# Performance work log

Hardware: AMD Instinct MI355X
Metric: run time of the kernel (lower is better)

## Reference

```python
import jax, jax.numpy as jnp
import numpy as np

# SwitchNet f* dims
B = 1024
Nb1, Nw1 = 8, 10          # input: Nb1^2=64 blocks, window 2*Nw1^2=200
Nb2x, Nb2y = 8, 8
Nw2x, Nw2y = 10, 10
R = 16
J1 = Nb1 * Nb1            # 64
K1 = 2 * Nw1 * Nw1        # 200
L1 = Nb2x * Nb2y * R      # 1024
J2 = Nb2x * Nb2y * J1     # 4096
J3 = Nb2x * Nb2y          # 64
K3 = J1 * R               # 1024
L3 = 2 * Nw2x * Nw2y      # 200


def _dm(x, kernel, bias):
    # per-block batched GEMM: x [B, J, K] @ kernel [J, K, L] + bias [1, J, L]
    return jnp.einsum('ijk,jkl->ijl', x, kernel) + bias


def setup_inputs() -> dict:
    key = jax.random.key(0)
    ks = jax.random.split(key, 7)
    u = lambda k, shape: jax.random.uniform(k, shape, dtype=jnp.float32) * 0.01
    return {
        'x': jax.random.normal(ks[0], (B, Nb1 * Nw1 * Nb1 * Nw1, 2), dtype=jnp.float32),
        'k1': u(ks[1], (J1, K1, L1)),
        'b1': u(ks[2], (1, J1, L1)),
        'k2': u(ks[3], (J2, R, R)),
        'b2': u(ks[4], (1, J2, R)),
        'k3': u(ks[5], (J3, K3, L3)),
        'b3': u(ks[6], (1, J3, L3)),
    }


def reference(x, k1, b1, k2, b2, k3, b3):
    bs = x.shape[0]
    # gather input windows: [B, Nb1, Nw1, Nb1, Nw1, 2] -> block-major
    h = x.reshape(bs, Nb1, Nw1, Nb1, Nw1, 2)
    h = h.transpose(0, 1, 3, 2, 4, 5)
    h = h.reshape(bs, J1, K1)
    h = _dm(h, k1, b1)                                   # [B, 64, 1024]
    h = h.reshape(bs, J1, Nb2x * Nb2y, R)
    h = h.transpose(0, 3, 1, 2)                          # [B, r, 64, 64]
    h = h.reshape(bs, J2, R)
    h = _dm(h, k2, b2)                                   # [B, 4096, r]
    h = h.reshape(bs, J3, K3)
    h = _dm(h, k3, b3)                                   # [B, 64, 200]
    h = h.reshape(bs, Nb2x, Nb2y, Nw2x, Nw2y, 2)
    h = h.transpose(0, 1, 3, 2, 4, 5)
    return h.reshape(bs, Nb2x * Nw2x, Nb2y * Nw2y, 2)   # [B, 80, 80, 2]
```

## Files before the change

kernel.cpp:

```cpp
#include <hip/hip_runtime.h>

typedef __attribute__((ext_vector_type(8))) short short8;
typedef __attribute__((ext_vector_type(4))) short bfx4;
typedef __attribute__((ext_vector_type(4))) float floatx4;

__device__ __forceinline__ float bf2f(short u) {
  unsigned int i = ((unsigned int)(unsigned short)u) << 16;
  return __builtin_bit_cast(float, i);
}
__device__ __forceinline__ short f2bf(float f) {
  unsigned int x = __builtin_bit_cast(unsigned int, f);
  x += 0x7fffu + ((x >> 16) & 1u);
  return (short)(x >> 16);
}

__device__ __forceinline__ void gl_lds16(const short* g, short* lds) {
  __builtin_amdgcn_global_load_lds(
      (const __attribute__((address_space(1))) unsigned int*)g,
      (__attribute__((address_space(3))) unsigned int*)lds, 16, 0, 0);
}

#define BC 256

__global__ __launch_bounds__(256) void gather_x(const float* __restrict__ x,
                                                short* __restrict__ hA, int bOffset) {
  int tid = blockIdx.x * 256 + threadIdx.x;
  const int total = 64 * BC * 112;
  if (tid >= total) return;
  int kp2 = tid % 112;
  int rem = tid / 112;
  int b_loc = rem & (BC - 1);
  int j1 = rem / BC;
  unsigned int pair = 0;
  if (kp2 < 100) {
    int wx = kp2 / 10;
    int wy = kp2 - wx * 10;
    int bx = j1 >> 3, by = j1 & 7;
    const float* p = x + (size_t)(bOffset + b_loc) * 12800 +
                     ((size_t)(bx * 800 + wx * 80 + by * 10 + wy)) * 2;
    float2 v = *(const float2*)p;
    pair = ((unsigned int)(unsigned short)f2bf(v.x)) |
           (((unsigned int)(unsigned short)f2bf(v.y)) << 16);
  }
  *(unsigned int*)&hA[rem * 224 + kp2 * 2] = pair;
}

__global__ __launch_bounds__(256) void transpose_k1(const float* __restrict__ k1,
                                                    short* __restrict__ k1t) {
  const int j1 = blockIdx.x;
  const int nBase = blockIdx.y * 64;
  const int kBase = blockIdx.z * 56;
  __shared__ short tr[64][68];
  const int t = threadIdx.x;
  const int nl = t & 63;
  const int ksub = t >> 6;
  const float* src = k1 + (size_t)j1 * 204800 + (size_t)kBase * 1024 + nBase + nl;
#pragma unroll
  for (int pass = 0; pass < 14; ++pass) {
    int kloc = pass * 4 + ksub;
    int k = kBase + kloc;
    tr[nl][kloc] = (k < 200) ? f2bf(src[kloc * 1024]) : (short)0;
  }
  __syncthreads();
  short* dstbase = k1t + ((size_t)j1 * 1024 + nBase) * 224 + kBase;
#pragma unroll
  for (int p = 0; p < 4; ++p) {
    int u = p * 256 + t;
    int row = u >> 4;
    int kq = u & 15;
    if (kq < 14) {
      bfx4 v = *(const bfx4*)&tr[row][kq * 4];
      *(bfx4*)&dstbase[row * 224 + kq * 4] = v;
    }
  }
}

__global__ __launch_bounds__(256) void transpose_k3(const float* __restrict__ k3,
                                                    short* __restrict__ k3t) {
  const int j3 = blockIdx.x;
  const int kBase = blockIdx.y * 128;
  const int nBase = blockIdx.z * 64;
  __shared__ short tr[64][132];
  const int t = threadIdx.x;
  const int nl = t & 63;
  const int ksub = t >> 6;
  const int nGlob = nBase + nl;
  const bool valid = (nGlob < 200);
  const float* src = k3 + (size_t)j3 * 204800 + (size_t)kBase * 200 + nGlob;
#pragma unroll 4
  for (int pass = 0; pass < 32; ++pass) {
    int k = pass * 4 + ksub;
    tr[nl][k] = valid ? f2bf(src[k * 200]) : (short)0;
  }
  __syncthreads();
  short* dstbase = k3t + ((size_t)j3 * 256 + nBase) * 1024 + kBase;
#pragma unroll
  for (int pass = 0; pass < 8; ++pass) {
    int idx = (pass * 256 + t) * 4;
    int row = idx >> 7;
    int koff = idx & 127;
    bfx4 v = *(const bfx4*)&tr[row][koff];
    *(bfx4*)&dstbase[row * 1024 + koff] = v;
  }
}

__global__ __launch_bounds__(256) void gemm_stage1(const short* __restrict__ hA,
                                                   const short* __restrict__ k1t,
                                                   const float* __restrict__ b1,
                                                   short* __restrict__ h1) {
  int bid = (int)blockIdx.x + 8 * (int)blockIdx.y + 16 * (int)blockIdx.z;
  bid = ((bid & 7) << 7) | (bid >> 3);
  const int nBase = (bid & 7) * 128;
  const int mBase = ((bid >> 3) & 1) * 128;
  const int j1 = bid >> 4;
  __shared__ short As[128 * 64];
  __shared__ short Bs[128 * 64];
  const int tid = threadIdx.x;
  const int lane = tid & 63;
  const int wave = tid >> 6;
  const int quad = lane >> 4;
  const int l16 = lane & 15;
  const int wm = wave >> 1, wn = wave & 1;
  const int sRow = tid >> 3;
  const int sCol = ((tid & 7) ^ (sRow & 7)) * 8;
  const short* Aj = hA + (size_t)j1 * BC * 224 + (size_t)(mBase + sRow) * 224 + sCol;
  const short* Bj =
      k1t + (size_t)j1 * 1024 * 224 + (size_t)(nBase + sRow) * 224 + sCol;
  const int tRow = tid >> 2;
  const int tCol = (tid & 3) * 8;
  const short* Ajt =
      hA + (size_t)j1 * BC * 224 + (size_t)(mBase + tRow) * 224 + 192 + tCol;
  const short* Bjt =
      k1t + (size_t)j1 * 1024 * 224 + (size_t)(nBase + tRow) * 224 + 192 + tCol;
  short* ldsA = &As[tid * 8];
  short* ldsB = &Bs[tid * 8];
  floatx4 acc[4][4] = {};

  for (int kk = 0; kk < 192; kk += 64) {
    __syncthreads();
#pragma unroll
    for (int c = 0; c < 4; ++c) {
      gl_lds16(Aj + c * 32 * 224 + kk, ldsA + c * 2048);
      gl_lds16(Bj + c * 32 * 224 + kk, ldsB + c * 2048);
    }
    __syncthreads();
#pragma unroll
    for (int ks = 0; ks < 2; ++ks) {
      short8 af[4], bfv[4];
#pragma unroll
      for (int mt = 0; mt < 4; ++mt) {
        int r = wm * 64 + mt * 16 + l16;
        af[mt] = *(const short8*)&As[r * 64 + ((ks * 4 + quad) ^ (l16 & 7)) * 8];
      }
#pragma unroll
      for (int nt = 0; nt < 4; ++nt) {
        int r = wn * 64 + nt * 16 + l16;
        bfv[nt] = *(const short8*)&Bs[r * 64 + ((ks * 4 + quad) ^ (l16 & 7)) * 8];
      }
#pragma unroll
      for (int mt = 0; mt < 4; ++mt)
#pragma unroll
        for (int nt = 0; nt < 4; ++nt)
          acc[mt][nt] = __builtin_amdgcn_mfma_f32_16x16x32_bf16(af[mt], bfv[nt],
                                                                acc[mt][nt], 0, 0, 0);
    }
  }
  __syncthreads();
  gl_lds16(Ajt, ldsA);
  gl_lds16(Ajt + 64 * 224, ldsA + 2048);
  gl_lds16(Bjt, ldsB);
  gl_lds16(Bjt + 64 * 224, ldsB + 2048);
  __syncthreads();
  {
    short8 af[4], bfv[4];
#pragma unroll
    for (int mt = 0; mt < 4; ++mt)
      af[mt] = *(const short8*)&As[(wm * 64 + mt * 16 + l16) * 32 + quad * 8];
#pragma unroll
    for (int nt = 0; nt < 4; ++nt)
      bfv[nt] = *(const short8*)&Bs[(wn * 64 + nt * 16 + l16) * 32 + quad * 8];
#pragma unroll
    for (int mt = 0; mt < 4; ++mt)
#pragma unroll
      for (int nt = 0; nt < 4; ++nt)
        acc[mt][nt] = __builtin_amdgcn_mfma_f32_16x16x32_bf16(af[mt], bfv[nt],
                                                              acc[mt][nt], 0, 0, 0);
  }
#pragma unroll
  for (int nt = 0; nt < 4; ++nt) {
    int n = nBase + wn * 64 + nt * 16 + l16;
    float bias = b1[j1 * 1024 + n];
#pragma unroll
    for (int mt = 0; mt < 4; ++mt) {
#pragma unroll
      for (int r = 0; r < 4; ++r) {
        int m = mBase + wm * 64 + mt * 16 + quad * 4 + r;
        h1[((size_t)j1 * BC + m) * 1024 + n] = f2bf(acc[mt][nt][r] + bias);
      }
    }
  }
}

__global__ __launch_bounds__(256) void stage2(const short* __restrict__ h1,
                                              const float* __restrict__ k2,
                                              const float* __restrict__ b2,
                                              short* __restrict__ h2p, int mTot,
                                              int bOff2) {
  const int j1 = blockIdx.x;
  const int bBase = blockIdx.y * 8;
  __shared__ short in_s[8][1024];
  __shared__ short w_s[256 * 66];
  __shared__ float bias_s[16 * 64];
  const int tid = threadIdx.x;
#pragma unroll
  for (int ii = 0; ii < 4; ++ii) {
    int flat = (ii * 256 + tid) * 8;
    int b_loc = flat >> 10;
    int k = flat & 1023;
    *(short8*)&in_s[b_loc][k] =
        *(const short8*)&h1[((size_t)j1 * BC + bBase + b_loc) * 1024 + k];
  }
#pragma unroll
  for (int ii = 0; ii < 16; ++ii) {
    int flat = (ii * 256 + tid) * 4;
    int blk = flat >> 8;
    int within = flat & 255;
    int r = blk >> 2, b2hi = blk & 3;
    int j2 = r * 256 + j1 * 4 + b2hi;
    floatx4 v = *(const floatx4*)&k2[(size_t)j2 * 256 + within];
#pragma unroll
    for (int i = 0; i < 4; ++i) w_s[(within + i) * 66 + blk] = f2bf(v[i]);
  }
  {
    int blk = tid >> 2;
    int r2o = (tid & 3) * 4;
    int r = blk >> 2, b2hi = blk & 3;
    int j2 = r * 256 + j1 * 4 + b2hi;
#pragma unroll
    for (int i = 0; i < 4; ++i) bias_s[(r2o + i) * 64 + blk] = b2[j2 * 16 + r2o + i];
  }
  __syncthreads();
#pragma unroll
  for (int i4 = 0; i4 < 2; ++i4) {
    int idx = i4 * 256 + tid;
    int b_loc = idx >> 6;
    int rem = idx & 63;
    int r = rem >> 2;
    int b2hi = rem & 3;
    float acc[16];
#pragma unroll
    for (int r2 = 0; r2 < 16; ++r2) acc[r2] = bias_s[r2 * 64 + rem];
#pragma unroll
    for (int k = 0; k < 16; ++k) {
      float iv = bf2f(in_s[b_loc][(b2hi * 16 + k) * 16 + r]);
#pragma unroll
      for (int r2 = 0; r2 < 16; ++r2)
        acc[r2] += iv * bf2f(w_s[(k * 16 + r2) * 66 + rem]);
    }
    int j3 = r * 4 + (j1 >> 4);
    int k3o = (j1 & 15) * 64 + b2hi * 16;
    short8 o0, o1;
#pragma unroll
    for (int t = 0; t < 8; ++t) {
      o0[t] = f2bf(acc[t]);
      o1[t] = f2bf(acc[8 + t]);
    }
    short* dst = h2p + ((size_t)j3 * mTot + bOff2 + bBase + b_loc) * 1024 + k3o;
    *(short8*)&dst[0] = o0;
    *(short8*)&dst[8] = o1;
  }
}

__global__ __launch_bounds__(256) void gemm_stage3(const short* __restrict__ h2p,
                                                   const short* __restrict__ k3t,
                                                   const float* __restrict__ b3,
                                                   float* __restrict__ out, int mTot,
                                                   int bOffset) {
  const int gy = (int)gridDim.y;
  int bid = (int)blockIdx.x + 2 * ((int)blockIdx.y + gy * (int)blockIdx.z);
  const int cpx = (gy << 4);
  bid = (bid & 7) * cpx + (bid >> 3);
  const int nBase = (bid & 1) * 128;
  const int rest = bid >> 1;
  const int mBase = (rest & (gy - 1)) * 128;
  const int j3 = rest / gy;
  __shared__ short As[128 * 64];
  __shared__ short Bs[128 * 64];
  const int tid = threadIdx.x;
  const int lane = tid & 63;
  const int wave = tid >> 6;
  const int quad = lane >> 4;
  const int l16 = lane & 15;
  const int wm = wave >> 1, wn = wave & 1;
  const int sRow = tid >> 3;
  const int sCol = ((tid & 7) ^ (sRow & 7)) * 8;
  const short* Aj =
      h2p + (size_t)j3 * mTot * 1024 + (size_t)(mBase + sRow) * 1024 + sCol;
  const short* Bj =
      k3t + (size_t)j3 * 256 * 1024 + (size_t)(nBase + sRow) * 1024 + sCol;
  short* ldsA = &As[tid * 8];
  short* ldsB = &Bs[tid * 8];
  floatx4 acc[4][4] = {};

  for (int kk = 0; kk < 1024; kk += 64) {
    __syncthreads();
#pragma unroll
    for (int c = 0; c < 4; ++c) {
      gl_lds16(Aj + c * 32 * 1024 + kk, ldsA + c * 2048);
      gl_lds16(Bj + c * 32 * 1024 + kk, ldsB + c * 2048);
    }
    __syncthreads();
#pragma unroll
    for (int ks = 0; ks < 2; ++ks) {
      short8 af[4], bfv[4];
#pragma unroll
      for (int mt = 0; mt < 4; ++mt) {
        int r = wm * 64 + mt * 16 + l16;
        af[mt] = *(const short8*)&As[r * 64 + ((ks * 4 + quad) ^ (l16 & 7)) * 8];
      }
#pragma unroll
      for (int nt = 0; nt < 4; ++nt) {
        int r = wn * 64 + nt * 16 + l16;
        bfv[nt] = *(const short8*)&Bs[r * 64 + ((ks * 4 + quad) ^ (l16 & 7)) * 8];
      }
#pragma unroll
      for (int mt = 0; mt < 4; ++mt)
#pragma unroll
        for (int nt = 0; nt < 4; ++nt)
          acc[mt][nt] = __builtin_amdgcn_mfma_f32_16x16x32_bf16(af[mt], bfv[nt],
                                                                acc[mt][nt], 0, 0, 0);
    }
  }
  const int B2x = j3 >> 3, B2y = j3 & 7;
#pragma unroll
  for (int nt = 0; nt < 4; ++nt) {
    int n = nBase + wn * 64 + nt * 16 + l16;
    if (n < 200) {
      float bias = b3[j3 * 200 + n];
      int c = n & 1;
      int t = n >> 1;
      int w2x = t / 10, w2y = t - w2x * 10;
      int orow = B2x * 10 + w2x, ocol = B2y * 10 + w2y;
#pragma unroll
      for (int mt = 0; mt < 4; ++mt) {
#pragma unroll
        for (int r = 0; r < 4; ++r) {
          int m = bOffset + mBase + wm * 64 + mt * 16 + quad * 4 + r;
          out[(((size_t)m * 80 + orow) * 80 + ocol) * 2 + c] = acc[mt][nt][r] + bias;
        }
      }
    }
  }
}

extern "C" void kernel_launch(void* const* d_in, const int* in_sizes, int n_in,
                              void* d_out, int out_size, void* d_ws, size_t ws_size,
                              hipStream_t stream) {
  const float* x = (const float*)d_in[0];
  const float* k1 = (const float*)d_in[1];
  const float* b1 = (const float*)d_in[2];
  const float* k2 = (const float*)d_in[3];
  const float* b2 = (const float*)d_in[4];
  const float* k3 = (const float*)d_in[5];
  const float* b3 = (const float*)d_in[6];
  float* out = (float*)d_out;
  char* ws = (char*)d_ws;

  short* k1t = (short*)(ws);
  short* k3t = (short*)(ws + 29360128);
  short* hA = (short*)(ws + 62914560);
  short* h1c = (short*)(ws + 70254592);
  short* h2p = (short*)(ws + 103809024);

  const bool full = (ws_size >= 238026752ull);
  const int mTot = full ? 1024 : BC;

  transpose_k1<<<dim3(64, 16, 4), 256, 0, stream>>>(k1, k1t);
  transpose_k3<<<dim3(64, 8, 4), 256, 0, stream>>>(k3, k3t);
  for (int c = 0; c < 1024 / BC; ++c) {
    int bOffset = c * BC;
    gather_x<<<(64 * BC * 112) / 256, 256, 0, stream>>>(x, hA, bOffset);
    gemm_stage1<<<dim3(8, BC / 128, 64), 256, 0, stream>>>(hA, k1t, b1, h1c);
    stage2<<<dim3(64, BC / 8), 256, 0, stream>>>(h1c, k2, b2, h2p, mTot,
                                                 full ? bOffset : 0);
    if (!full)
      gemm_stage3<<<dim3(2, BC / 128, 64), 256, 0, stream>>>(h2p, k3t, b3, out, BC,
                                                             bOffset);
  }
  if (full)
    gemm_stage3<<<dim3(2, 1024 / 128, 64), 256, 0, stream>>>(h2p, k3t, b3, out, 1024,
                                                             0);
}
```

Before: 534.2 us.

## Restructure stage2 with register tiling, direct-to-LDS loads, and block swizzle

Stage2 now processes 16 batch rows per block instead of 8, loading the h1 tile with global_load_lds and repacking k2 into a vectorizable short8 layout in LDS. Each thread computes an 8x8 register tile (8 batch rows by 8 outputs), reusing each weight vector across rows, and reads bias straight from global memory. A block-index swizzle groups blocks for locality. The aim is fewer LDS reads per FMA and half as many weight reloads, at the cost of more registers (64 accumulators) and a larger LDS footprint.

```diff
diff --git a/kernel.cpp b/kernel.cpp
--- a/kernel.cpp
+++ b/kernel.cpp
@@ -206,68 +206,84 @@
                                               const float* __restrict__ b2,
                                               short* __restrict__ h2p, int mTot,
                                               int bOff2) {
-  const int j1 = blockIdx.x;
-  const int bBase = blockIdx.y * 8;
-  __shared__ short in_s[8][1024];
-  __shared__ short w_s[256 * 66];
-  __shared__ float bias_s[16 * 64];
+  int bid = (int)blockIdx.x + 64 * (int)blockIdx.y;
+  bid = ((bid & 7) << 7) | (bid >> 3);
+  const int j1 = bid >> 4;
+  const int bBase = (bid & 15) * 16;
+  __shared__ short in_s[16 * 1024];
+  __shared__ short w_s[16 * 1024];
   const int tid = threadIdx.x;
-#pragma unroll
-  for (int ii = 0; ii < 4; ++ii) {
-    int flat = (ii * 256 + tid) * 8;
-    int b_loc = flat >> 10;
-    int k = flat & 1023;
-    *(short8*)&in_s[b_loc][k] =
-        *(const short8*)&h1[((size_t)j1 * BC + bBase + b_loc) * 1024 + k];
-  }
-#pragma unroll
-  for (int ii = 0; ii < 16; ++ii) {
-    int flat = (ii * 256 + tid) * 4;
-    int blk = flat >> 8;
-    int within = flat & 255;
-    int r = blk >> 2, b2hi = blk & 3;
-    int j2 = r * 256 + j1 * 4 + b2hi;
-    floatx4 v = *(const floatx4*)&k2[(size_t)j2 * 256 + within];
-#pragma unroll
-    for (int i = 0; i < 4; ++i) w_s[(within + i) * 66 + blk] = f2bf(v[i]);
-  }
+
+  const short* inSrc = h1 + ((size_t)j1 * BC + bBase) * 1024 + tid * 8;
+  short* inDst = &in_s[tid * 8];
+#pragma unroll
+  for (int c = 0; c < 8; ++c) gl_lds16(inSrc + c * 2048, inDst + c * 2048);
+
+#pragma unroll
+  for (int p = 0; p < 8; ++p) {
+    int idx = p * 256 + tid;
+    int rm = idx & 63;
+    int g = (idx >> 6) & 1;
+    int k = idx >> 7;
+    int j2s = (rm >> 2) * 256 + j1 * 4 + (rm & 3);
+    const float* s = &k2[(size_t)j2s * 256 + k * 16 + g * 8];
+    floatx4 v0 = *(const floatx4*)s;
+    floatx4 v1 = *(const floatx4*)(s + 4);
+    short8 w;
+#pragma unroll
+    for (int i = 0; i < 4; ++i) {
+      w[i] = f2bf(v0[i]);
+      w[4 + i] = f2bf(v1[i]);
+    }
+    *(short8*)&w_s[idx * 8] = w;
+  }
+  __syncthreads();
+
+  const int rem = tid & 63;
+  const int oct = tid >> 6;
+  const int bh = oct & 1;
+  const int ro = oct >> 1;
+  const int r = rem >> 2, b2hi = rem & 3;
+  const int j2 = r * 256 + j1 * 4 + b2hi;
+
+  float acc[8][8];
   {
-    int blk = tid >> 2;
-    int r2o = (tid & 3) * 4;
-    int r = blk >> 2, b2hi = blk & 3;
-    int j2 = r * 256 + j1 * 4 + b2hi;
-#pragma unroll
-    for (int i = 0; i < 4; ++i) bias_s[(r2o + i) * 64 + blk] = b2[j2 * 16 + r2o + i];
-  }
-  __syncthreads();
-#pragma unroll
-  for (int i4 = 0; i4 < 2; ++i4) {
-    int idx = i4 * 256 + tid;
-    int b_loc = idx >> 6;
-    int rem = idx & 63;
-    int r = rem >> 2;
-    int b2hi = rem & 3;
-    float acc[16];
-#pragma unroll
-    for (int r2 = 0; r2 < 16; ++r2) acc[r2] = bias_s[r2 * 64 + rem];
-#pragma unroll
-    for (int k = 0; k < 16; ++k) {
-      float iv = bf2f(in_s[b_loc][(b2hi * 16 + k) * 16 + r]);
-#pragma unroll
-      for (int r2 = 0; r2 < 16; ++r2)
-        acc[r2] += iv * bf2f(w_s[(k * 16 + r2) * 66 + rem]);
-    }
-    int j3 = r * 4 + (j1 >> 4);
-    int k3o = (j1 & 15) * 64 + b2hi * 16;
-    short8 o0, o1;
-#pragma unroll
-    for (int t = 0; t < 8; ++t) {
-      o0[t] = f2bf(acc[t]);
-      o1[t] = f2bf(acc[8 + t]);
-    }
-    short* dst = h2p + ((size_t)j3 * mTot + bOff2 + bBase + b_loc) * 1024 + k3o;
-    *(short8*)&dst[0] = o0;
-    *(short8*)&dst[8] = o1;
+    const float* bb = &b2[(size_t)j2 * 16 + ro * 8];
+    floatx4 bz0 = *(const floatx4*)bb;
+    floatx4 bz1 = *(const floatx4*)(bb + 4);
+#pragma unroll
+    for (int b = 0; b < 8; ++b)
+#pragma unroll
+      for (int j = 0; j < 4; ++j) {
+        acc[b][j] = bz0[j];
+        acc[b][4 + j] = bz1[j];
+      }
+  }
+  const short* inb = &in_s[(bh * 8) * 1024 + (b2hi * 16) * 16 + r];
+  const short* wb = &w_s[(ro * 64 + rem) * 8];
+#pragma unroll
+  for (int k = 0; k < 16; ++k) {
+    short8 w8 = *(const short8*)&wb[k * 1024];
+    float wf[8];
+#pragma unroll
+    for (int j = 0; j < 8; ++j) wf[j] = bf2f(w8[j]);
+#pragma unroll
+    for (int b = 0; b < 8; ++b) {
+      float iv = bf2f(inb[b * 1024 + k * 16]);
+#pragma unroll
+      for (int j = 0; j < 8; ++j) acc[b][j] += iv * wf[j];
+    }
+  }
+  const int j3 = r * 4 + (j1 >> 4);
+  const int k3o = (j1 & 15) * 64 + b2hi * 16 + ro * 8;
+#pragma unroll
+  for (int b = 0; b < 8; ++b) {
+    short8 o;
+#pragma unroll
+    for (int j = 0; j < 8; ++j) o[j] = f2bf(acc[b][j]);
+    short* dst =
+        h2p + ((size_t)j3 * mTot + bOff2 + bBase + bh * 8 + b) * 1024 + k3o;
+    *(short8*)dst = o;
   }
 }
 
@@ -381,8 +397,8 @@
     int bOffset = c * BC;
     gather_x<<<(64 * BC * 112) / 256, 256, 0, stream>>>(x, hA, bOffset);
     gemm_stage1<<<dim3(8, BC / 128, 64), 256, 0, stream>>>(hA, k1t, b1, h1c);
-    stage2<<<dim3(64, BC / 8), 256, 0, stream>>>(h1c, k2, b2, h2p, mTot,
-                                                 full ? bOffset : 0);
+    stage2<<<dim3(64, BC / 16), 256, 0, stream>>>(h1c, k2, b2, h2p, mTot,
+                                                  full ? bOffset : 0);
     if (!full)
       gemm_stage3<<<dim3(2, BC / 128, 64), 256, 0, stream>>>(h2p, k3t, b3, out, BC,
                                                              bOffset);
```

Result: faster. 480.0 us, median of 2 (-10.2%).
